# Optimization experiments

Hardware: AMD Instinct MI355X
Metric: run time of the kernel (lower is better)

Reference implementation:

```python
import jax, jax.numpy as jnp
import numpy as np

H = 16  # num heads

def setup_inputs() -> dict:
    key = jax.random.key(0)
    k1, k2, k3 = jax.random.split(key, 3)
    B, L, D = 2, 2048, 1024
    x = jax.random.normal(k1, (B, L, D), dtype=jnp.float32)
    # torch Linear weight is [out,in]; we store transposed [in,out] so y = x @ W
    w_qkv = jax.random.normal(k2, (D, 3 * D), dtype=jnp.float32) * (D ** -0.5)
    w_proj = jax.random.normal(k3, (D, D), dtype=jnp.float32) * (D ** -0.5)
    return {"x": x, "w_qkv": w_qkv, "w_proj": w_proj, "num_prefix_tokens": 256}

def _prefix_causal_mask(L: int, M: int):
    # True = masked. Strict upper triangle (causal), then text rows (M:) may
    # see ALL prefix columns (:M).
    mask = jnp.triu(jnp.ones((L, L), dtype=bool), k=1)
    mask = mask.at[M:, :M].set(False)
    return mask

def reference(x, w_qkv, w_proj, num_prefix_tokens):
    B, L, D = x.shape
    d = D // H
    scale = d ** -0.5
    qkv = (x @ w_qkv).reshape(B, L, 3, H, d)
    q = jnp.transpose(qkv[:, :, 0], (0, 2, 1, 3))  # [B,H,L,d]
    k = jnp.transpose(qkv[:, :, 1], (0, 2, 1, 3))
    v = jnp.transpose(qkv[:, :, 2], (0, 2, 1, 3))
    logits = jnp.einsum("bhqd,bhkd->bhqk", q, k) * scale  # [B,H,L,L]
    mask = _prefix_causal_mask(L, num_prefix_tokens)
    logits = jnp.where(mask[None, None], -jnp.inf, logits)
    attn = jax.nn.softmax(logits, axis=-1)
    out = jnp.einsum("bhqk,bhkd->bhqd", attn, v)  # [B,H,L,d]
    out = jnp.transpose(out, (0, 2, 1, 3)).reshape(B, L, D)
    return out @ w_proj
```

## Files before the change

### kernel.cpp

```cpp
#include <hip/hip_runtime.h>
#include <hip/hip_bf16.h>

#define BATCH   2
#define L_SEQ   2048
#define DMODEL  1024
#define NHEADS  16
#define DHEAD   64
#define SEG     (BATCH*NHEADS*L_SEQ*DHEAD)

typedef __attribute__((ext_vector_type(8))) short bf16x8;
typedef __attribute__((ext_vector_type(4))) float f32x4;

__device__ __forceinline__ unsigned short f2b(float f) {
    unsigned int u = __float_as_uint(f);
    return (unsigned short)((u + 0x7FFFu + ((u >> 16) & 1u)) >> 16);
}
__device__ __forceinline__ unsigned int pk2(float a, float b) {
    __hip_bfloat162 h = __float22bfloat162_rn(make_float2(a, b));
    return *(unsigned int*)&h;
}

__global__ __launch_bounds__(256)
void cast_bf16(const float* __restrict__ in, unsigned short* __restrict__ out, int n) {
    int i = (blockIdx.x * 256 + threadIdx.x) * 4;
    if (i < n) {
        float4 f = *(const float4*)&in[i];
        ushort4 o;
        o.x = f2b(f.x); o.y = f2b(f.y); o.z = f2b(f.z); o.w = f2b(f.w);
        *(ushort4*)&out[i] = o;
    }
}

__global__ __launch_bounds__(256)
void transpose_cast(const float* __restrict__ in, unsigned short* __restrict__ out,
                    int K, int N) {
    __shared__ unsigned short T[64][65];
    const int k0 = blockIdx.y * 64, n0 = blockIdx.x * 64;
    const int t = threadIdx.x;
    const int r = t >> 4, c4 = (t & 15) * 4;
#pragma unroll
    for (int rep = 0; rep < 4; ++rep) {
        int kk = rep * 16 + r;
        float4 f = *(const float4*)&in[(size_t)(k0 + kk) * N + n0 + c4];
        T[kk][c4 + 0] = f2b(f.x);
        T[kk][c4 + 1] = f2b(f.y);
        T[kk][c4 + 2] = f2b(f.z);
        T[kk][c4 + 3] = f2b(f.w);
    }
    __syncthreads();
#pragma unroll
    for (int rep = 0; rep < 4; ++rep) {
        int nn = rep * 16 + r;
        ushort4 o;
        o.x = T[c4 + 0][nn];
        o.y = T[c4 + 1][nn];
        o.z = T[c4 + 2][nn];
        o.w = T[c4 + 3][nn];
        *(ushort4*)&out[(size_t)(n0 + nn) * K + k0 + c4] = o;
    }
}

template <int MODE>
__global__ __launch_bounds__(256)
void gemm_bf16(const unsigned short* __restrict__ A, const unsigned short* __restrict__ Bt,
               float* __restrict__ Cf, unsigned short* __restrict__ Cb,
               int M, int K, int N) {
    __shared__ unsigned short Asm[128 * 40];
    __shared__ unsigned short Bsm[128 * 40];

    const int t = threadIdx.x;
    const int lane = t & 63, wave = t >> 6;
    const int quad = lane >> 4, l16 = lane & 15;
    const int wm = (wave >> 1) * 64, wn = (wave & 1) * 64;
    const int m0 = blockIdx.y * 128, n0 = blockIdx.x * 128;
    const int srow = t >> 2, sc = (t & 3) * 8;

    f32x4 acc[4][4];
#pragma unroll
    for (int i = 0; i < 4; ++i)
#pragma unroll
        for (int j = 0; j < 4; ++j)
#pragma unroll
            for (int r = 0; r < 4; ++r) acc[i][j][r] = 0.0f;

    bf16x8 ga0 = *(const bf16x8*)&A[(size_t)(m0 + srow) * K + sc];
    bf16x8 ga1 = *(const bf16x8*)&A[(size_t)(m0 + srow + 64) * K + sc];
    bf16x8 gb0 = *(const bf16x8*)&Bt[(size_t)(n0 + srow) * K + sc];
    bf16x8 gb1 = *(const bf16x8*)&Bt[(size_t)(n0 + srow + 64) * K + sc];

    for (int k0 = 0; k0 < K; k0 += 32) {
        __syncthreads();
        *(bf16x8*)&Asm[srow * 40 + sc] = ga0;
        *(bf16x8*)&Asm[(srow + 64) * 40 + sc] = ga1;
        *(bf16x8*)&Bsm[srow * 40 + sc] = gb0;
        *(bf16x8*)&Bsm[(srow + 64) * 40 + sc] = gb1;
        if (k0 + 32 < K) {
            ga0 = *(const bf16x8*)&A[(size_t)(m0 + srow) * K + k0 + 32 + sc];
            ga1 = *(const bf16x8*)&A[(size_t)(m0 + srow + 64) * K + k0 + 32 + sc];
            gb0 = *(const bf16x8*)&Bt[(size_t)(n0 + srow) * K + k0 + 32 + sc];
            gb1 = *(const bf16x8*)&Bt[(size_t)(n0 + srow + 64) * K + k0 + 32 + sc];
        }
        __syncthreads();
        bf16x8 af[4], bfr[4];
#pragma unroll
        for (int i = 0; i < 4; ++i)
            af[i] = *(const bf16x8*)&Asm[(wm + i * 16 + l16) * 40 + quad * 8];
#pragma unroll
        for (int j = 0; j < 4; ++j)
            bfr[j] = *(const bf16x8*)&Bsm[(wn + j * 16 + l16) * 40 + quad * 8];
#pragma unroll
        for (int i = 0; i < 4; ++i)
#pragma unroll
            for (int j = 0; j < 4; ++j)
                acc[i][j] = __builtin_amdgcn_mfma_f32_16x16x32_bf16(af[i], bfr[j], acc[i][j], 0, 0, 0);
    }

    if (MODE == 0) {
#pragma unroll
        for (int i = 0; i < 4; ++i)
#pragma unroll
            for (int r = 0; r < 4; ++r) {
                int row = m0 + wm + i * 16 + quad * 4 + r;
#pragma unroll
                for (int j = 0; j < 4; ++j) {
                    int col = n0 + wn + j * 16 + l16;
                    Cf[(size_t)row * N + col] = acc[i][j][r];
                }
            }
    } else {
        const float qscale = 0.1803368801111244f;
#pragma unroll
        for (int j = 0; j < 4; ++j) {
            int n = n0 + wn + j * 16 + l16;
            int s = n >> 10, h = (n >> 6) & 15, dd = n & 63;
            if (s == 2) {
#pragma unroll
                for (int i = 0; i < 4; ++i) {
                    int row0 = m0 + wm + i * 16 + quad * 4;
                    int b = row0 >> 11, lpos = row0 & (L_SEQ - 1);
                    unsigned int w0 = pk2(acc[i][j][0], acc[i][j][1]);
                    unsigned int w1 = pk2(acc[i][j][2], acc[i][j][3]);
                    size_t dst = 2 * (size_t)SEG +
                                 (((size_t)(b * NHEADS + h) * DHEAD + dd) * L_SEQ) + lpos;
                    *(uint2*)&Cb[dst] = make_uint2(w0, w1);
                }
            } else {
                float scl = (s == 0) ? qscale : 1.0f;
#pragma unroll
                for (int i = 0; i < 4; ++i)
#pragma unroll
                    for (int r = 0; r < 4; ++r) {
                        int row = m0 + wm + i * 16 + quad * 4 + r;
                        int b = row >> 11, lpos = row & (L_SEQ - 1);
                        size_t dst = (size_t)s * SEG +
                                     (((size_t)(b * NHEADS + h) * L_SEQ + lpos) * DHEAD) + dd;
                        Cb[dst] = f2b(acc[i][j][r] * scl);
                    }
            }
        }
    }
}

__global__ __launch_bounds__(256)
void attn_mfma(const unsigned short* __restrict__ Qg, const unsigned short* __restrict__ Kg,
               const unsigned short* __restrict__ Vg, unsigned short* __restrict__ Ao) {
    __shared__ unsigned short Ksm[64 * 72];
    __shared__ unsigned short Vsm[64 * 72];
    __shared__ unsigned short Psm[64 * 72];

    const int t = threadIdx.x;
    const int lane = t & 63, wave = t >> 6;
    const int quad = lane >> 4, l16 = lane & 15;
    const int bh = blockIdx.x & 31;
    const int u = blockIdx.x >> 5, v = u & 7, g = u >> 3;
    const int qt = (g == 0) ? 31 - v : (g == 1) ? 16 + v : (g == 2) ? 15 - v : v;
    const int q0 = qt * 64;
    const size_t qkbase = (size_t)bh * L_SEQ * DHEAD;
    const size_t vbase  = (size_t)bh * DHEAD * L_SEQ;
    const int sr = t >> 3, sc8 = (t & 7) * 8;

    bf16x8 bq0 = *(const bf16x8*)&Qg[qkbase + (size_t)(q0 + wave * 16 + l16) * DHEAD + quad * 8];
    bf16x8 bq1 = *(const bf16x8*)&Qg[qkbase + (size_t)(q0 + wave * 16 + l16) * DHEAD + 32 + quad * 8];

    f32x4 o[4];
#pragma unroll
    for (int nt = 0; nt < 4; ++nt)
#pragma unroll
        for (int r = 0; r < 4; ++r) o[nt][r] = 0.0f;
    float m_st = -1e30f, l_st = 0.0f;

    bf16x8 gk0 = *(const bf16x8*)&Kg[qkbase + (size_t)sr * DHEAD + sc8];
    bf16x8 gk1 = *(const bf16x8*)&Kg[qkbase + (size_t)(sr + 32) * DHEAD + sc8];
    bf16x8 gv0 = *(const bf16x8*)&Vg[vbase + (size_t)sr * L_SEQ + sc8];
    bf16x8 gv1 = *(const bf16x8*)&Vg[vbase + (size_t)(sr + 32) * L_SEQ + sc8];

    for (int kt = 0; kt <= qt; ++kt) {
        __syncthreads();
        *(bf16x8*)&Ksm[sr * 72 + sc8] = gk0;
        *(bf16x8*)&Ksm[(sr + 32) * 72 + sc8] = gk1;
        *(bf16x8*)&Vsm[sr * 72 + sc8] = gv0;
        *(bf16x8*)&Vsm[(sr + 32) * 72 + sc8] = gv1;
        if (kt < qt) {
            const int kn = (kt + 1) * 64;
            gk0 = *(const bf16x8*)&Kg[qkbase + (size_t)(kn + sr) * DHEAD + sc8];
            gk1 = *(const bf16x8*)&Kg[qkbase + (size_t)(kn + sr + 32) * DHEAD + sc8];
            gv0 = *(const bf16x8*)&Vg[vbase + (size_t)sr * L_SEQ + kn + sc8];
            gv1 = *(const bf16x8*)&Vg[vbase + (size_t)(sr + 32) * L_SEQ + kn + sc8];
        }
        __syncthreads();

        f32x4 ST[4];
#pragma unroll
        for (int nt = 0; nt < 4; ++nt) {
            bf16x8 a0 = *(const bf16x8*)&Ksm[(nt * 16 + l16) * 72 + quad * 8];
            bf16x8 a1 = *(const bf16x8*)&Ksm[(nt * 16 + l16) * 72 + 32 + quad * 8];
            f32x4 z;
#pragma unroll
            for (int r = 0; r < 4; ++r) z[r] = 0.0f;
            z = __builtin_amdgcn_mfma_f32_16x16x32_bf16(a0, bq0, z, 0, 0, 0);
            ST[nt] = __builtin_amdgcn_mfma_f32_16x16x32_bf16(a1, bq1, z, 0, 0, 0);
        }

        if (kt == qt) {
            const int qloc = wave * 16 + l16;
#pragma unroll
            for (int nt = 0; nt < 4; ++nt)
#pragma unroll
                for (int r = 0; r < 4; ++r)
                    if (nt * 16 + quad * 4 + r > qloc) ST[nt][r] = -1e30f;
        }

        float mx = ST[0][0];
#pragma unroll
        for (int nt = 0; nt < 4; ++nt)
#pragma unroll
            for (int r = 0; r < 4; ++r) mx = fmaxf(mx, ST[nt][r]);
        mx = fmaxf(mx, __shfl_xor(mx, 16, 64));
        mx = fmaxf(mx, __shfl_xor(mx, 32, 64));
        float mn = fmaxf(m_st, mx);
        float alpha = __builtin_amdgcn_exp2f(m_st - mn);
        m_st = mn;

        float rs = 0.0f;
        unsigned int pw[4][2];
#pragma unroll
        for (int nt = 0; nt < 4; ++nt) {
            float p0 = __builtin_amdgcn_exp2f(ST[nt][0] - mn);
            float p1 = __builtin_amdgcn_exp2f(ST[nt][1] - mn);
            float p2 = __builtin_amdgcn_exp2f(ST[nt][2] - mn);
            float p3 = __builtin_amdgcn_exp2f(ST[nt][3] - mn);
            pw[nt][0] = pk2(p0, p1);
            pw[nt][1] = pk2(p2, p3);
            rs += (p0 + p1) + (p2 + p3);
        }
        rs += __shfl_xor(rs, 16, 64);
        rs += __shfl_xor(rs, 32, 64);
        l_st = l_st * alpha + rs;

#pragma unroll
        for (int nt = 0; nt < 4; ++nt)
            *(uint2*)&Psm[(wave * 16 + l16) * 72 + nt * 16 + quad * 4] =
                make_uint2(pw[nt][0], pw[nt][1]);

        float alC[4];
#pragma unroll
        for (int r = 0; r < 4; ++r) alC[r] = __shfl(alpha, quad * 4 + r, 16);
#pragma unroll
        for (int nt = 0; nt < 4; ++nt)
#pragma unroll
            for (int r = 0; r < 4; ++r) o[nt][r] *= alC[r];

        bf16x8 ap0 = *(const bf16x8*)&Psm[(wave * 16 + l16) * 72 + quad * 8];
        bf16x8 ap1 = *(const bf16x8*)&Psm[(wave * 16 + l16) * 72 + 32 + quad * 8];
#pragma unroll
        for (int nt = 0; nt < 4; ++nt) {
            bf16x8 b0 = *(const bf16x8*)&Vsm[(nt * 16 + l16) * 72 + quad * 8];
            bf16x8 b1 = *(const bf16x8*)&Vsm[(nt * 16 + l16) * 72 + 32 + quad * 8];
            o[nt] = __builtin_amdgcn_mfma_f32_16x16x32_bf16(ap0, b0, o[nt], 0, 0, 0);
            o[nt] = __builtin_amdgcn_mfma_f32_16x16x32_bf16(ap1, b1, o[nt], 0, 0, 0);
        }
    }

    float linv = 1.0f / l_st;
    float lC[4];
#pragma unroll
    for (int r = 0; r < 4; ++r) lC[r] = __shfl(linv, quad * 4 + r, 16);
    const int b = bh >> 4, h = bh & 15;
#pragma unroll
    for (int r = 0; r < 4; ++r) {
        int row = q0 + wave * 16 + quad * 4 + r;
        size_t ob = ((size_t)(b * L_SEQ + row)) * DMODEL + h * DHEAD;
#pragma unroll
        for (int nt = 0; nt < 4; ++nt)
            Ao[ob + nt * 16 + l16] = f2b(o[nt][r] * lC[r]);
    }
}

extern "C" void kernel_launch(void* const* d_in, const int* in_sizes, int n_in,
                              void* d_out, int out_size, void* d_ws, size_t ws_size,
                              hipStream_t stream) {
    const float* x      = (const float*)d_in[0];
    const float* w_qkv  = (const float*)d_in[1];
    const float* w_proj = (const float*)d_in[2];
    float* out = (float*)d_out;

    unsigned short* ws     = (unsigned short*)d_ws;
    unsigned short* xb     = ws;
    unsigned short* wqkvT  = xb + 4194304;
    unsigned short* wprojT = wqkvT + 3145728;
    unsigned short* qkv    = wprojT + 1048576;
    unsigned short* ao     = qkv + 3 * (size_t)SEG;

    const int M = BATCH * L_SEQ;

    cast_bf16<<<4096, 256, 0, stream>>>(x, xb, M * DMODEL);
    transpose_cast<<<dim3(48, 16), 256, 0, stream>>>(w_qkv, wqkvT, DMODEL, 3 * DMODEL);
    transpose_cast<<<dim3(16, 16), 256, 0, stream>>>(w_proj, wprojT, DMODEL, DMODEL);

    gemm_bf16<1><<<dim3(24, 32), 256, 0, stream>>>(xb, wqkvT, nullptr, qkv, M, DMODEL, 3 * DMODEL);

    attn_mfma<<<BATCH * NHEADS * (L_SEQ / 64), 256, 0, stream>>>(
        qkv, qkv + SEG, qkv + 2 * (size_t)SEG, ao);

    gemm_bf16<0><<<dim3(8, 32), 256, 0, stream>>>(ao, wprojT, out, nullptr, M, DMODEL, DMODEL);
}
```

Before: 190.5 us.

## Use direct global-to-LDS loads with XOR swizzle in GEMM and pair attention q-tiles

The GEMM now loads 64-wide K tiles straight into LDS with global_load_lds and an XOR-swizzled layout instead of padded register staging. This removes the register round trip and padding, but the prefetch-overlap pipeline is gone. The attention kernel also uses swizzled unpadded LDS and has each block process a complementary pair of query tiles (31-p and p) for balanced causal work over 512 blocks. Its softmax uses the previous running max (lagged rescale), moving the max reduction off the critical path before the exponentials.

```diff
diff --git a/kernel.cpp b/kernel.cpp
--- a/kernel.cpp
+++ b/kernel.cpp
@@ -18,6 +18,11 @@
 __device__ __forceinline__ unsigned int pk2(float a, float b) {
     __hip_bfloat162 h = __float22bfloat162_rn(make_float2(a, b));
     return *(unsigned int*)&h;
+}
+__device__ __forceinline__ void glds16(const unsigned short* g, unsigned short* l) {
+    __builtin_amdgcn_global_load_lds(
+        (const __attribute__((address_space(1))) unsigned int*)g,
+        (__attribute__((address_space(3))) unsigned int*)l, 16, 0, 0);
 }
 
 __global__ __launch_bounds__(256)
@@ -65,15 +70,29 @@
 void gemm_bf16(const unsigned short* __restrict__ A, const unsigned short* __restrict__ Bt,
                float* __restrict__ Cf, unsigned short* __restrict__ Cb,
                int M, int K, int N) {
-    __shared__ unsigned short Asm[128 * 40];
-    __shared__ unsigned short Bsm[128 * 40];
+    __shared__ unsigned short Asm[128 * 64];
+    __shared__ unsigned short Bsm[128 * 64];
 
     const int t = threadIdx.x;
     const int lane = t & 63, wave = t >> 6;
     const int quad = lane >> 4, l16 = lane & 15;
     const int wm = (wave >> 1) * 64, wn = (wave & 1) * 64;
     const int m0 = blockIdx.y * 128, n0 = blockIdx.x * 128;
-    const int srow = t >> 2, sc = (t & 3) * 8;
+
+    const int gsw = (lane & 7) ^ (lane >> 3);
+    const unsigned short* ga[4];
+    const unsigned short* gb[4];
+    unsigned short* la[4];
+    unsigned short* lb[4];
+#pragma unroll
+    for (int i = 0; i < 4; ++i) {
+        int row = wave * 32 + i * 8 + (lane >> 3);
+        ga[i] = &A[(size_t)(m0 + row) * K + gsw * 8];
+        gb[i] = &Bt[(size_t)(n0 + row) * K + gsw * 8];
+        la[i] = &Asm[(wave * 32 + i * 8) * 64];
+        lb[i] = &Bsm[(wave * 32 + i * 8) * 64];
+    }
+    const int sx = l16 & 7;
 
     f32x4 acc[4][4];
 #pragma unroll
@@ -83,36 +102,29 @@
 #pragma unroll
             for (int r = 0; r < 4; ++r) acc[i][j][r] = 0.0f;
 
-    bf16x8 ga0 = *(const bf16x8*)&A[(size_t)(m0 + srow) * K + sc];
-    bf16x8 ga1 = *(const bf16x8*)&A[(size_t)(m0 + srow + 64) * K + sc];
-    bf16x8 gb0 = *(const bf16x8*)&Bt[(size_t)(n0 + srow) * K + sc];
-    bf16x8 gb1 = *(const bf16x8*)&Bt[(size_t)(n0 + srow + 64) * K + sc];
-
-    for (int k0 = 0; k0 < K; k0 += 32) {
+    for (int k0 = 0; k0 < K; k0 += 64) {
         __syncthreads();
-        *(bf16x8*)&Asm[srow * 40 + sc] = ga0;
-        *(bf16x8*)&Asm[(srow + 64) * 40 + sc] = ga1;
-        *(bf16x8*)&Bsm[srow * 40 + sc] = gb0;
-        *(bf16x8*)&Bsm[(srow + 64) * 40 + sc] = gb1;
-        if (k0 + 32 < K) {
-            ga0 = *(const bf16x8*)&A[(size_t)(m0 + srow) * K + k0 + 32 + sc];
-            ga1 = *(const bf16x8*)&A[(size_t)(m0 + srow + 64) * K + k0 + 32 + sc];
-            gb0 = *(const bf16x8*)&Bt[(size_t)(n0 + srow) * K + k0 + 32 + sc];
-            gb1 = *(const bf16x8*)&Bt[(size_t)(n0 + srow + 64) * K + k0 + 32 + sc];
+#pragma unroll
+        for (int i = 0; i < 4; ++i) {
+            glds16(ga[i] + k0, la[i]);
+            glds16(gb[i] + k0, lb[i]);
         }
         __syncthreads();
-        bf16x8 af[4], bfr[4];
-#pragma unroll
-        for (int i = 0; i < 4; ++i)
-            af[i] = *(const bf16x8*)&Asm[(wm + i * 16 + l16) * 40 + quad * 8];
-#pragma unroll
-        for (int j = 0; j < 4; ++j)
-            bfr[j] = *(const bf16x8*)&Bsm[(wn + j * 16 + l16) * 40 + quad * 8];
-#pragma unroll
-        for (int i = 0; i < 4; ++i)
+#pragma unroll
+        for (int s = 0; s < 2; ++s) {
+            bf16x8 af[4], bfr[4];
+#pragma unroll
+            for (int i = 0; i < 4; ++i)
+                af[i] = *(const bf16x8*)&Asm[(wm + i * 16 + l16) * 64 + ((4 * s + quad) ^ sx) * 8];
 #pragma unroll
             for (int j = 0; j < 4; ++j)
-                acc[i][j] = __builtin_amdgcn_mfma_f32_16x16x32_bf16(af[i], bfr[j], acc[i][j], 0, 0, 0);
+                bfr[j] = *(const bf16x8*)&Bsm[(wn + j * 16 + l16) * 64 + ((4 * s + quad) ^ sx) * 8];
+#pragma unroll
+            for (int i = 0; i < 4; ++i)
+#pragma unroll
+                for (int j = 0; j < 4; ++j)
+                    acc[i][j] = __builtin_amdgcn_mfma_f32_16x16x32_bf16(af[i], bfr[j], acc[i][j], 0, 0, 0);
+        }
     }
 
     if (MODE == 0) {
@@ -164,135 +176,152 @@
 __global__ __launch_bounds__(256)
 void attn_mfma(const unsigned short* __restrict__ Qg, const unsigned short* __restrict__ Kg,
                const unsigned short* __restrict__ Vg, unsigned short* __restrict__ Ao) {
-    __shared__ unsigned short Ksm[64 * 72];
-    __shared__ unsigned short Vsm[64 * 72];
-    __shared__ unsigned short Psm[64 * 72];
+    __shared__ unsigned short Ksm[64 * 64];
+    __shared__ unsigned short Vsm[64 * 64];
+    __shared__ unsigned short Psm[64 * 64];
 
     const int t = threadIdx.x;
     const int lane = t & 63, wave = t >> 6;
     const int quad = lane >> 4, l16 = lane & 15;
-    const int bh = blockIdx.x & 31;
-    const int u = blockIdx.x >> 5, v = u & 7, g = u >> 3;
-    const int qt = (g == 0) ? 31 - v : (g == 1) ? 16 + v : (g == 2) ? 15 - v : v;
-    const int q0 = qt * 64;
+    const int bh = blockIdx.x & 31, p = blockIdx.x >> 5;
     const size_t qkbase = (size_t)bh * L_SEQ * DHEAD;
     const size_t vbase  = (size_t)bh * DHEAD * L_SEQ;
-    const int sr = t >> 3, sc8 = (t & 7) * 8;
-
-    bf16x8 bq0 = *(const bf16x8*)&Qg[qkbase + (size_t)(q0 + wave * 16 + l16) * DHEAD + quad * 8];
-    bf16x8 bq1 = *(const bf16x8*)&Qg[qkbase + (size_t)(q0 + wave * 16 + l16) * DHEAD + 32 + quad * 8];
-
-    f32x4 o[4];
-#pragma unroll
-    for (int nt = 0; nt < 4; ++nt)
-#pragma unroll
-        for (int r = 0; r < 4; ++r) o[nt][r] = 0.0f;
-    float m_st = -1e30f, l_st = 0.0f;
-
-    bf16x8 gk0 = *(const bf16x8*)&Kg[qkbase + (size_t)sr * DHEAD + sc8];
-    bf16x8 gk1 = *(const bf16x8*)&Kg[qkbase + (size_t)(sr + 32) * DHEAD + sc8];
-    bf16x8 gv0 = *(const bf16x8*)&Vg[vbase + (size_t)sr * L_SEQ + sc8];
-    bf16x8 gv1 = *(const bf16x8*)&Vg[vbase + (size_t)(sr + 32) * L_SEQ + sc8];
-
-    for (int kt = 0; kt <= qt; ++kt) {
-        __syncthreads();
-        *(bf16x8*)&Ksm[sr * 72 + sc8] = gk0;
-        *(bf16x8*)&Ksm[(sr + 32) * 72 + sc8] = gk1;
-        *(bf16x8*)&Vsm[sr * 72 + sc8] = gv0;
-        *(bf16x8*)&Vsm[(sr + 32) * 72 + sc8] = gv1;
-        if (kt < qt) {
-            const int kn = (kt + 1) * 64;
-            gk0 = *(const bf16x8*)&Kg[qkbase + (size_t)(kn + sr) * DHEAD + sc8];
-            gk1 = *(const bf16x8*)&Kg[qkbase + (size_t)(kn + sr + 32) * DHEAD + sc8];
-            gv0 = *(const bf16x8*)&Vg[vbase + (size_t)sr * L_SEQ + kn + sc8];
-            gv1 = *(const bf16x8*)&Vg[vbase + (size_t)(sr + 32) * L_SEQ + kn + sc8];
-        }
-        __syncthreads();
-
-        f32x4 ST[4];
-#pragma unroll
-        for (int nt = 0; nt < 4; ++nt) {
-            bf16x8 a0 = *(const bf16x8*)&Ksm[(nt * 16 + l16) * 72 + quad * 8];
-            bf16x8 a1 = *(const bf16x8*)&Ksm[(nt * 16 + l16) * 72 + 32 + quad * 8];
-            f32x4 z;
-#pragma unroll
-            for (int r = 0; r < 4; ++r) z[r] = 0.0f;
-            z = __builtin_amdgcn_mfma_f32_16x16x32_bf16(a0, bq0, z, 0, 0, 0);
-            ST[nt] = __builtin_amdgcn_mfma_f32_16x16x32_bf16(a1, bq1, z, 0, 0, 0);
-        }
-
-        if (kt == qt) {
-            const int qloc = wave * 16 + l16;
+    const int b = bh >> 4, h = bh & 15;
+
+    const int r0 = t >> 3, c0 = t & 7;
+    const int sw = c0 ^ (r0 & 7);
+    const int ls0 = r0 * 64 + c0 * 8, ls1 = (r0 + 32) * 64 + c0 * 8;
+    const int sx = l16 & 7;
+
+    bf16x8 gk0, gk1, gv0, gv1;
+    gk0 = *(const bf16x8*)&Kg[qkbase + (size_t)r0 * DHEAD + sw * 8];
+    gk1 = *(const bf16x8*)&Kg[qkbase + (size_t)(r0 + 32) * DHEAD + sw * 8];
+    gv0 = *(const bf16x8*)&Vg[vbase + (size_t)r0 * L_SEQ + sw * 8];
+    gv1 = *(const bf16x8*)&Vg[vbase + (size_t)(r0 + 32) * L_SEQ + sw * 8];
+
+#pragma unroll
+    for (int half = 0; half < 2; ++half) {
+        const int qt = (half == 0) ? (31 - p) : p;
+        const int q0 = qt * 64;
+        const int nkt = qt + 1;
+
+        const size_t qrow = qkbase + (size_t)(q0 + wave * 16 + l16) * DHEAD;
+        bf16x8 bq0 = *(const bf16x8*)&Qg[qrow + quad * 8];
+        bf16x8 bq1 = *(const bf16x8*)&Qg[qrow + 32 + quad * 8];
+
+        f32x4 o[4];
+#pragma unroll
+        for (int nt = 0; nt < 4; ++nt)
+#pragma unroll
+            for (int r = 0; r < 4; ++r) o[nt][r] = 0.0f;
+        float m_used = 0.0f, rs = 0.0f, alphaB = 1.0f;
+        float alC[4] = {1.0f, 1.0f, 1.0f, 1.0f};
+
+        for (int kt = 0; kt < nkt; ++kt) {
+            __syncthreads();
+            *(bf16x8*)&Ksm[ls0] = gk0;
+            *(bf16x8*)&Ksm[ls1] = gk1;
+            *(bf16x8*)&Vsm[ls0] = gv0;
+            *(bf16x8*)&Vsm[ls1] = gv1;
+            if (kt + 1 < nkt) {
+                const int kn = (kt + 1) * 64;
+                gk0 = *(const bf16x8*)&Kg[qkbase + (size_t)(kn + r0) * DHEAD + sw * 8];
+                gk1 = *(const bf16x8*)&Kg[qkbase + (size_t)(kn + r0 + 32) * DHEAD + sw * 8];
+                gv0 = *(const bf16x8*)&Vg[vbase + (size_t)r0 * L_SEQ + kn + sw * 8];
+                gv1 = *(const bf16x8*)&Vg[vbase + (size_t)(r0 + 32) * L_SEQ + kn + sw * 8];
+            } else if (half == 0) {
+                gk0 = *(const bf16x8*)&Kg[qkbase + (size_t)r0 * DHEAD + sw * 8];
+                gk1 = *(const bf16x8*)&Kg[qkbase + (size_t)(r0 + 32) * DHEAD + sw * 8];
+                gv0 = *(const bf16x8*)&Vg[vbase + (size_t)r0 * L_SEQ + sw * 8];
+                gv1 = *(const bf16x8*)&Vg[vbase + (size_t)(r0 + 32) * L_SEQ + sw * 8];
+            }
+            __syncthreads();
+
+            f32x4 ST[4];
+#pragma unroll
+            for (int nt = 0; nt < 4; ++nt) {
+                bf16x8 a0 = *(const bf16x8*)&Ksm[(nt * 16 + l16) * 64 + ((quad) ^ sx) * 8];
+                bf16x8 a1 = *(const bf16x8*)&Ksm[(nt * 16 + l16) * 64 + ((4 + quad) ^ sx) * 8];
+                f32x4 z;
+#pragma unroll
+                for (int r = 0; r < 4; ++r) z[r] = 0.0f;
+                z = __builtin_amdgcn_mfma_f32_16x16x32_bf16(a0, bq0, z, 0, 0, 0);
+                ST[nt] = __builtin_amdgcn_mfma_f32_16x16x32_bf16(a1, bq1, z, 0, 0, 0);
+            }
+
+            if (kt == nkt - 1) {
+                const int qloc = wave * 16 + l16;
+#pragma unroll
+                for (int nt = 0; nt < 4; ++nt)
+#pragma unroll
+                    for (int r = 0; r < 4; ++r)
+                        if (nt * 16 + quad * 4 + r > qloc) ST[nt][r] = -1e30f;
+            }
+
+            rs *= alphaB;
 #pragma unroll
             for (int nt = 0; nt < 4; ++nt)
 #pragma unroll
-                for (int r = 0; r < 4; ++r)
-                    if (nt * 16 + quad * 4 + r > qloc) ST[nt][r] = -1e30f;
-        }
-
-        float mx = ST[0][0];
-#pragma unroll
-        for (int nt = 0; nt < 4; ++nt)
-#pragma unroll
-            for (int r = 0; r < 4; ++r) mx = fmaxf(mx, ST[nt][r]);
-        mx = fmaxf(mx, __shfl_xor(mx, 16, 64));
-        mx = fmaxf(mx, __shfl_xor(mx, 32, 64));
-        float mn = fmaxf(m_st, mx);
-        float alpha = __builtin_amdgcn_exp2f(m_st - mn);
-        m_st = mn;
-
-        float rs = 0.0f;
-        unsigned int pw[4][2];
-#pragma unroll
-        for (int nt = 0; nt < 4; ++nt) {
-            float p0 = __builtin_amdgcn_exp2f(ST[nt][0] - mn);
-            float p1 = __builtin_amdgcn_exp2f(ST[nt][1] - mn);
-            float p2 = __builtin_amdgcn_exp2f(ST[nt][2] - mn);
-            float p3 = __builtin_amdgcn_exp2f(ST[nt][3] - mn);
-            pw[nt][0] = pk2(p0, p1);
-            pw[nt][1] = pk2(p2, p3);
-            rs += (p0 + p1) + (p2 + p3);
-        }
-        rs += __shfl_xor(rs, 16, 64);
-        rs += __shfl_xor(rs, 32, 64);
-        l_st = l_st * alpha + rs;
-
-#pragma unroll
-        for (int nt = 0; nt < 4; ++nt)
-            *(uint2*)&Psm[(wave * 16 + l16) * 72 + nt * 16 + quad * 4] =
-                make_uint2(pw[nt][0], pw[nt][1]);
-
-        float alC[4];
-#pragma unroll
-        for (int r = 0; r < 4; ++r) alC[r] = __shfl(alpha, quad * 4 + r, 16);
-#pragma unroll
-        for (int nt = 0; nt < 4; ++nt)
-#pragma unroll
-            for (int r = 0; r < 4; ++r) o[nt][r] *= alC[r];
-
-        bf16x8 ap0 = *(const bf16x8*)&Psm[(wave * 16 + l16) * 72 + quad * 8];
-        bf16x8 ap1 = *(const bf16x8*)&Psm[(wave * 16 + l16) * 72 + 32 + quad * 8];
-#pragma unroll
-        for (int nt = 0; nt < 4; ++nt) {
-            bf16x8 b0 = *(const bf16x8*)&Vsm[(nt * 16 + l16) * 72 + quad * 8];
-            bf16x8 b1 = *(const bf16x8*)&Vsm[(nt * 16 + l16) * 72 + 32 + quad * 8];
-            o[nt] = __builtin_amdgcn_mfma_f32_16x16x32_bf16(ap0, b0, o[nt], 0, 0, 0);
-            o[nt] = __builtin_amdgcn_mfma_f32_16x16x32_bf16(ap1, b1, o[nt], 0, 0, 0);
-        }
-    }
-
-    float linv = 1.0f / l_st;
-    float lC[4];
-#pragma unroll
-    for (int r = 0; r < 4; ++r) lC[r] = __shfl(linv, quad * 4 + r, 16);
-    const int b = bh >> 4, h = bh & 15;
-#pragma unroll
-    for (int r = 0; r < 4; ++r) {
-        int row = q0 + wave * 16 + quad * 4 + r;
-        size_t ob = ((size_t)(b * L_SEQ + row)) * DMODEL + h * DHEAD;
-#pragma unroll
-        for (int nt = 0; nt < 4; ++nt)
-            Ao[ob + nt * 16 + l16] = f2b(o[nt][r] * lC[r]);
+                for (int r = 0; r < 4; ++r) o[nt][r] *= alC[r];
+
+            float tm = -1e30f, add = 0.0f;
+            unsigned int pw[4][2];
+#pragma unroll
+            for (int nt = 0; nt < 4; ++nt) {
+                float p0 = __builtin_amdgcn_exp2f(ST[nt][0] - m_used);
+                float p1 = __builtin_amdgcn_exp2f(ST[nt][1] - m_used);
+                float p2 = __builtin_amdgcn_exp2f(ST[nt][2] - m_used);
+                float p3 = __builtin_amdgcn_exp2f(ST[nt][3] - m_used);
+                tm = fmaxf(tm, fmaxf(fmaxf(ST[nt][0], ST[nt][1]), fmaxf(ST[nt][2], ST[nt][3])));
+                pw[nt][0] = pk2(p0, p1);
+                pw[nt][1] = pk2(p2, p3);
+                add += (p0 + p1) + (p2 + p3);
+            }
+            rs += add;
+
+            {
+                const int prow = wave * 16 + l16;
+                const int pc = (quad >> 1), po = (quad & 1) * 4;
+#pragma unroll
+                for (int nt = 0; nt < 4; ++nt)
+                    *(uint2*)&Psm[prow * 64 + ((2 * nt + pc) ^ (prow & 7)) * 8 + po] =
+                        make_uint2(pw[nt][0], pw[nt][1]);
+            }
+
+            bf16x8 ap0 = *(const bf16x8*)&Psm[(wave * 16 + l16) * 64 + ((quad) ^ sx) * 8];
+            bf16x8 ap1 = *(const bf16x8*)&Psm[(wave * 16 + l16) * 64 + ((4 + quad) ^ sx) * 8];
+#pragma unroll
+            for (int nt = 0; nt < 4; ++nt) {
+                bf16x8 b0 = *(const bf16x8*)&Vsm[(nt * 16 + l16) * 64 + ((quad) ^ sx) * 8];
+                bf16x8 b1 = *(const bf16x8*)&Vsm[(nt * 16 + l16) * 64 + ((4 + quad) ^ sx) * 8];
+                o[nt] = __builtin_amdgcn_mfma_f32_16x16x32_bf16(ap0, b0, o[nt], 0, 0, 0);
+                o[nt] = __builtin_amdgcn_mfma_f32_16x16x32_bf16(ap1, b1, o[nt], 0, 0, 0);
+            }
+
+            tm = fmaxf(tm, __shfl_xor(tm, 16, 64));
+            tm = fmaxf(tm, __shfl_xor(tm, 32, 64));
+            float m_next = fmaxf(m_used, tm);
+            alphaB = __builtin_amdgcn_exp2f(m_used - m_next);
+#pragma unroll
+            for (int r = 0; r < 4; ++r) alC[r] = __shfl(alphaB, quad * 4 + r, 16);
+            m_used = m_next;
+        }
+
+        float l = rs;
+        l += __shfl_xor(l, 16, 64);
+        l += __shfl_xor(l, 32, 64);
+        float linv = 1.0f / l;
+        float lC[4];
+#pragma unroll
+        for (int r = 0; r < 4; ++r) lC[r] = __shfl(linv, quad * 4 + r, 16);
+#pragma unroll
+        for (int r = 0; r < 4; ++r) {
+            int row = q0 + wave * 16 + quad * 4 + r;
+            size_t ob = ((size_t)(b * L_SEQ + row)) * DMODEL + h * DHEAD;
+#pragma unroll
+            for (int nt = 0; nt < 4; ++nt)
+                Ao[ob + nt * 16 + l16] = f2b(o[nt][r] * lC[r]);
+        }
     }
 }
 
@@ -319,8 +348,7 @@
 
     gemm_bf16<1><<<dim3(24, 32), 256, 0, stream>>>(xb, wqkvT, nullptr, qkv, M, DMODEL, 3 * DMODEL);
 
-    attn_mfma<<<BATCH * NHEADS * (L_SEQ / 64), 256, 0, stream>>>(
-        qkv, qkv + SEG, qkv + 2 * (size_t)SEG, ao);
+    attn_mfma<<<512, 256, 0, stream>>>(qkv, qkv + SEG, qkv + 2 * (size_t)SEG, ao);
 
     gemm_bf16<0><<<dim3(8, 32), 256, 0, stream>>>(ao, wprojT, out, nullptr, M, DMODEL, DMODEL);
 }
```

New measurement: 183.8 us. 1.04x faster.
